# Kernel tuning notes

Hardware: AMD Instinct MI355X
Metric: run time of the kernel (lower is better)

The kernel has to match this reference:

```python
import jax, jax.numpy as jnp
import numpy as np

LN_EPS = 1e-5
MIN_BW, MAX_BW, BW_FACTOR = 0.1, 10.0, 1.0
BETA = 0.1


def _layernorm(h, g, b):
    mu = jnp.mean(h, axis=-1, keepdims=True)
    var = jnp.mean((h - mu) ** 2, axis=-1, keepdims=True)
    return (h - mu) * jax.lax.rsqrt(var + LN_EPS) * g + b


def _mlp(x, W1, b1, g, beta, W2, b2):
    # Linear -> LayerNorm -> Dropout(eval: identity) -> GELU(exact) -> Linear
    h = x @ W1 + b1
    h = _layernorm(h, g, beta)
    h = jax.nn.gelu(h, approximate=False)
    return h @ W2 + b2


def _normalize(x):
    n = jnp.linalg.norm(x, axis=-1, keepdims=True)
    return x / jnp.maximum(n, 1e-12)


def _bandwidth(x, y):
    # median-heuristic bandwidth on up to 512 samples; no grad through it
    s = min(512, x.shape[0])
    xs, ys = x[:s], y[:s]
    diff = xs[:, None, :] - ys[None, :, :]          # [s, s, K]
    dist_sq = jnp.sum(diff ** 2, axis=-1)
    bw = jnp.sqrt(jnp.median(dist_sq.reshape(-1)) / 2.0) * BW_FACTOR
    return jax.lax.stop_gradient(jnp.clip(bw, MIN_BW, MAX_BW))


def _score_kernel(x, sx, y, sy):
    # 3-term KSD kernel matrix [B, B]
    bw = _bandwidth(x, y)
    bw2 = bw ** 2
    x2 = jnp.sum(x ** 2, axis=-1)
    y2 = jnp.sum(y ** 2, axis=-1)
    dist_sq = jnp.maximum(x2[:, None] + y2[None, :] - 2.0 * (x @ y.T), 0.0)
    k = jnp.exp(-dist_sq / (2.0 * bw2))
    term1 = k * (sx @ sy.T)
    # sum_d (x_i - y_j)_d * sy_jd  = x_i . sy_j - y_j . sy_j
    term2 = (x @ sy.T - jnp.sum(y * sy, axis=-1)[None, :]) * k / bw2
    D = x.shape[-1]
    term3 = dist_sq * k / (bw2 ** 2) - k * D / bw2
    return term1 + term2 + term3


def setup_inputs() -> dict:
    key = jax.random.key(0)
    B, L, D1, H, K = 256, 128, 768, 1024, 256
    ks = jax.random.split(key, 16)

    def w(k, shape):
        return (jax.random.normal(k, shape, dtype=jnp.float32) * 0.02)

    inp = {
        'image_features': jax.random.normal(ks[0], (B, L, D1), dtype=jnp.float32),
        'text_features': jax.random.normal(ks[1], (B, L, D1), dtype=jnp.float32),
        'eps_img': jax.random.normal(ks[2], (B, L, K), dtype=jnp.float32),
        'eps_txt': jax.random.normal(ks[3], (B, L, K), dtype=jnp.float32),
        'attention_mask': jnp.ones((B, L), dtype=jnp.int32),
    }
    # encoders: D1 -> H -> 2K ; score nets: K -> 2K -> K
    for pfx, k1, k2 in (('enc_i', ks[4], ks[5]), ('enc_t', ks[6], ks[7])):
        inp[pfx + '_W1'] = w(k1, (D1, H)); inp[pfx + '_b1'] = jnp.zeros((H,), jnp.float32)
        inp[pfx + '_g'] = jnp.ones((H,), jnp.float32); inp[pfx + '_beta'] = jnp.zeros((H,), jnp.float32)
        inp[pfx + '_W2'] = w(k2, (H, 2 * K)); inp[pfx + '_b2'] = jnp.zeros((2 * K,), jnp.float32)
    for pfx, k1, k2 in (('sc_i', ks[8], ks[9]), ('sc_t', ks[10], ks[11])):
        inp[pfx + '_W1'] = w(k1, (K, 2 * K)); inp[pfx + '_b1'] = jnp.zeros((2 * K,), jnp.float32)
        inp[pfx + '_g'] = jnp.ones((2 * K,), jnp.float32); inp[pfx + '_beta'] = jnp.zeros((2 * K,), jnp.float32)
        inp[pfx + '_W2'] = w(k2, (2 * K, K)); inp[pfx + '_b2'] = jnp.zeros((K,), jnp.float32)
    return inp


def reference(image_features, text_features, attention_mask, eps_img, eps_txt,
              enc_i_W1, enc_i_b1, enc_i_g, enc_i_beta, enc_i_W2, enc_i_b2,
              enc_t_W1, enc_t_b1, enc_t_g, enc_t_beta, enc_t_W2, enc_t_b2,
              sc_i_W1, sc_i_b1, sc_i_g, sc_i_beta, sc_i_W2, sc_i_b2,
              sc_t_W1, sc_t_b1, sc_t_g, sc_t_beta, sc_t_W2, sc_t_b2):
    B = image_features.shape[0]
    img_params = _mlp(image_features, enc_i_W1, enc_i_b1, enc_i_g, enc_i_beta, enc_i_W2, enc_i_b2)
    txt_params = _mlp(text_features, enc_t_W1, enc_t_b1, enc_t_g, enc_t_beta, enc_t_W2, enc_t_b2)
    K = img_params.shape[-1] // 2
    img_mu, img_logvar = img_params[..., :K], img_params[..., K:]
    txt_mu, txt_logvar = txt_params[..., :K], txt_params[..., K:]

    img_z = _normalize(img_mu + eps_img * jnp.exp(0.5 * img_logvar))
    txt_z = _normalize(txt_mu + eps_txt * jnp.exp(0.5 * txt_logvar))

    img_score = _mlp(img_z, sc_i_W1, sc_i_b1, sc_i_g, sc_i_beta, sc_i_W2, sc_i_b2)
    txt_score = _mlp(txt_z, sc_t_W1, sc_t_b1, sc_t_g, sc_t_beta, sc_t_W2, sc_t_b2)

    seq_last = jnp.sum(attention_mask, axis=1).astype(jnp.int32) - 1   # [B]
    bidx = jnp.arange(B)
    xz, yz = img_z[bidx, seq_last], txt_z[bidx, seq_last]
    xs, ys = img_score[bidx, seq_last], txt_score[bidx, seq_last]

    alignment_loss = jnp.mean(_score_kernel(xz, xs, yz, ys))

    kl1 = -0.5 * jnp.sum(1.0 + img_logvar - img_mu ** 2 - jnp.exp(img_logvar), axis=-1)
    kl2 = -0.5 * jnp.sum(1.0 + txt_logvar - txt_mu ** 2 - jnp.exp(txt_logvar), axis=-1)
    kl_loss = (jnp.mean(kl1[bidx, seq_last]) + jnp.mean(kl2[bidx, seq_last])) / 2.0

    total_loss = kl_loss + BETA * alignment_loss
    return total_loss
```

## Files before the change

### kernel.cpp

```cpp
#include <hip/hip_runtime.h>
#include <math.h>

#define Bb   256
#define Lq   128
#define D1   768
#define Hh   1024
#define Kk   256
#define K2v  512

#define OFF_EPSG  0
#define OFF_P     131072
#define OFF_Z     2228224
#define OFF_SCORE 2359296
#define OFF_DIST  2490368
#define OFF_HIST  2555904
#define OFF_SCAL  2564096
#define OFF_YSY   2564104
#define OFF_SEQL  2564616
#define OFF_BF    2564880

#define UB_XG   0
#define UB_HACT 393216
#define UB_ZB   917504
#define UB_WT   1048576
#define WT_EW1I 0
#define WT_EW1T 786432
#define WT_EW2I 1572864
#define WT_EW2T 2097152
#define WT_SW1I 2621440
#define WT_SW1T 2752512
#define WT_SW2I 2883584
#define WT_SW2T 3014656

typedef __attribute__((ext_vector_type(8))) short short8v;
typedef __attribute__((ext_vector_type(4))) float f32x4;

__device__ __forceinline__ float wred(float v){
#pragma unroll
  for (int m = 32; m; m >>= 1) v += __shfl_xor(v, m, 64);
  return v;
}
__device__ __forceinline__ float gelu_exact(float x){
  return 0.5f * x * (1.0f + erff(x * 0.70710678118654752f));
}
__device__ __forceinline__ ushort f2b(float f){
  union { float f; unsigned u; } v; v.f = f;
  return (ushort)((v.u + 0x7FFFu + ((v.u >> 16) & 1u)) >> 16);
}

__global__ __launch_bounds__(256) void k_init(const int* __restrict__ mask,
                                              int* __restrict__ seql,
                                              int* __restrict__ ghist,
                                              float* __restrict__ scal){
  const int t = threadIdx.x, b = blockIdx.x;
  if (b == 0){
    const int4* m4 = reinterpret_cast<const int4*>(mask + t * Lq);
    int s = 0;
#pragma unroll
    for (int i = 0; i < Lq/4; i++){ int4 v = m4[i]; s += v.x + v.y + v.z + v.w; }
    seql[t] = s - 1;
  } else {
    reinterpret_cast<int4*>(ghist)[(b-1)*256 + t] = make_int4(0,0,0,0);
    if (b == 1 && t < 8) scal[t] = 0.0f;
  }
}

__global__ __launch_bounds__(256) void k_gather_conv(
    const float* __restrict__ img, const float* __restrict__ txt,
    const float* __restrict__ epsi, const float* __restrict__ epst,
    const int* __restrict__ seql,
    const float* __restrict__ eW1i, const float* __restrict__ eW1t,
    const float* __restrict__ eW2i, const float* __restrict__ eW2t,
    const float* __restrict__ sW1i, const float* __restrict__ sW1t,
    const float* __restrict__ sW2i, const float* __restrict__ sW2t,
    ushort* __restrict__ xgb, float* __restrict__ epsg, ushort* __restrict__ wt)
{
  __shared__ float lsf[32][33];
  const int bid = blockIdx.x, t = threadIdx.x;
  if (bid < 256){
    const int b = bid, last = seql[b];
    const float4* ir = reinterpret_cast<const float4*>(img + (size_t)(b*Lq+last)*D1);
    const float4* tr = reinterpret_cast<const float4*>(txt + (size_t)(b*Lq+last)*D1);
    if (t < 192){
      float4 v = ir[t];
      ushort4 o; o.x=f2b(v.x); o.y=f2b(v.y); o.z=f2b(v.z); o.w=f2b(v.w);
      reinterpret_cast<ushort4*>(xgb + (size_t)b*D1)[t] = o;
      float4 w = tr[t];
      ushort4 p; p.x=f2b(w.x); p.y=f2b(w.y); p.z=f2b(w.z); p.w=f2b(w.w);
      reinterpret_cast<ushort4*>(xgb + (size_t)(Bb+b)*D1)[t] = p;
    }
    if (t < 64){
      reinterpret_cast<float4*>(epsg + (size_t)b*Kk)[t] =
        reinterpret_cast<const float4*>(epsi + (size_t)(b*Lq+last)*Kk)[t];
      reinterpret_cast<float4*>(epsg + (size_t)(Bb+b)*Kk)[t] =
        reinterpret_cast<const float4*>(epst + (size_t)(b*Lq+last)*Kk)[t];
    }
    return;
  }
  const int wb = bid - 256;
  const float* src; ushort* dst; int Kd, Nd, ti;
  if      (wb < 768){  src=eW1i; dst=wt+WT_EW1I; Kd=768;  Nd=1024; ti=wb; }
  else if (wb < 1536){ src=eW1t; dst=wt+WT_EW1T; Kd=768;  Nd=1024; ti=wb-768; }
  else if (wb < 2048){ src=eW2i; dst=wt+WT_EW2I; Kd=1024; Nd=512;  ti=wb-1536; }
  else if (wb < 2560){ src=eW2t; dst=wt+WT_EW2T; Kd=1024; Nd=512;  ti=wb-2048; }
  else if (wb < 2688){ src=sW1i; dst=wt+WT_SW1I; Kd=256;  Nd=512;  ti=wb-2560; }
  else if (wb < 2816){ src=sW1t; dst=wt+WT_SW1T; Kd=256;  Nd=512;  ti=wb-2688; }
  else if (wb < 2944){ src=sW2i; dst=wt+WT_SW2I; Kd=512;  Nd=256;  ti=wb-2816; }
  else               { src=sW2t; dst=wt+WT_SW2T; Kd=512;  Nd=256;  ti=wb-2944; }
  const int ntile = Nd / 32;
  const int k0 = (ti / ntile) * 32, n0 = (ti % ntile) * 32;
  const int r = t >> 3, q = t & 7;
  float4 v = reinterpret_cast<const float4*>(src + (size_t)(k0+r)*Nd + n0)[q];
  lsf[r][q*4+0]=v.x; lsf[r][q*4+1]=v.y; lsf[r][q*4+2]=v.z; lsf[r][q*4+3]=v.w;
  __syncthreads();
  ushort4 o;
  o.x = f2b(lsf[q*4+0][r]); o.y = f2b(lsf[q*4+1][r]);
  o.z = f2b(lsf[q*4+2][r]); o.w = f2b(lsf[q*4+3][r]);
  *reinterpret_cast<ushort4*>(dst + (size_t)(n0+r)*Kd + k0 + q*4) = o;
}

template<int BM, int KCH, int N, int K>
__global__ __launch_bounds__(256) void k_mgemm(
    const ushort* __restrict__ A, const ushort* __restrict__ WTi,
    const ushort* __restrict__ WTt, float* __restrict__ P)
{
  constexpr int RPW = BM / 64;
  __shared__ ushort LS[(BM + 64) * 32];
  const int tid = threadIdx.x;
  const int lane = tid & 63, wid = tid >> 6;
  const int n0 = blockIdx.x * 64;
  const int r0 = blockIdx.y * BM;
  const int kb = blockIdx.z * KCH;
  const ushort* WT = (r0 >= 256) ? WTt : WTi;

  f32x4 acc[RPW][4];
#pragma unroll
  for (int s = 0; s < RPW; s++)
#pragma unroll
    for (int c = 0; c < 4; c++) acc[s][c] = (f32x4){0.f,0.f,0.f,0.f};

  const int l15 = lane & 15, kg = lane >> 4;
  const int rdswz = (kg * 16) ^ ((l15 & 3) << 4);

  for (int k0 = kb; k0 < kb + KCH; k0 += 32){
    __syncthreads();
    constexpr int NCHK = (BM + 64) * 4;
#pragma unroll
    for (int i = 0; i < NCHK / 256; i++){
      const int q = (i * 256 + tid) * 16;
      const int row = q >> 6, koff = q & 63;
      const ushort* src = (row < BM)
          ? (A  + (size_t)(r0 + row) * K + k0)
          : (WT + (size_t)(n0 + row - BM) * K + k0);
      short8v v = *reinterpret_cast<const short8v*>(
          reinterpret_cast<const char*>(src) + koff);
      const int dq = (q & ~63) | (koff ^ ((row & 3) << 4));
      *reinterpret_cast<short8v*>(reinterpret_cast<char*>(LS) + dq) = v;
    }
    __syncthreads();
    const char* Ab = reinterpret_cast<const char*>(LS);
    const char* Bbp = reinterpret_cast<const char*>(LS + BM * 32);
    short8v ar[RPW], bc[4];
#pragma unroll
    for (int s = 0; s < RPW; s++){
      const int row = wid * (RPW * 16) + s * 16 + l15;
      ar[s] = *reinterpret_cast<const short8v*>(Ab + row * 64 + rdswz);
    }
#pragma unroll
    for (int c = 0; c < 4; c++){
      const int col = c * 16 + l15;
      bc[c] = *reinterpret_cast<const short8v*>(Bbp + col * 64 + rdswz);
    }
#pragma unroll
    for (int s = 0; s < RPW; s++)
#pragma unroll
      for (int c = 0; c < 4; c++)
        acc[s][c] = __builtin_amdgcn_mfma_f32_16x16x32_bf16(ar[s], bc[c], acc[s][c], 0, 0, 0);
  }
  const int ks = blockIdx.z;
#pragma unroll
  for (int s = 0; s < RPW; s++)
#pragma unroll
    for (int c = 0; c < 4; c++)
#pragma unroll
      for (int r = 0; r < 4; r++){
        const int row = r0 + wid * (RPW * 16) + s * 16 + kg * 4 + r;
        const int col = n0 + c * 16 + l15;
        P[((size_t)ks * 512 + row) * N + col] = acc[s][c][r];
      }
}

__global__ __launch_bounds__(256) void k_ln1(
    const float* __restrict__ P,
    const float* __restrict__ b1i, const float* __restrict__ b1t,
    const float* __restrict__ gi,  const float* __restrict__ gt,
    const float* __restrict__ bei, const float* __restrict__ bet,
    ushort* __restrict__ hb)
{
  __shared__ float2 wsum[4];
  const int row = blockIdx.x, t = threadIdx.x;
  const float* b1 = row >= 256 ? b1t : b1i;
  const float* g  = row >= 256 ? gt  : gi;
  const float* be = row >= 256 ? bet : bei;
  const float4* P4 = reinterpret_cast<const float4*>(P);
  float4 v = make_float4(0,0,0,0);
#pragma unroll
  for (int s = 0; s < 4; s++){
    float4 p = P4[((size_t)s * 512 + row) * (Hh/4) + t];
    v.x += p.x; v.y += p.y; v.z += p.z; v.w += p.w;
  }
  float4 bb = reinterpret_cast<const float4*>(b1)[t];
  v.x += bb.x; v.y += bb.y; v.z += bb.z; v.w += bb.w;
  float ps = wred(v.x + v.y + v.z + v.w);
  float pq = wred(v.x*v.x + v.y*v.y + v.z*v.z + v.w*v.w);
  if (!(t & 63)) wsum[t >> 6] = make_float2(ps, pq);
  __syncthreads();
  float S = 0, Q = 0;
#pragma unroll
  for (int i = 0; i < 4; i++){ S += wsum[i].x; Q += wsum[i].y; }
  float mean = S * (1.0f/Hh);
  float rstd = rsqrtf(Q * (1.0f/Hh) - mean*mean + 1e-5f);
  float4 gv  = reinterpret_cast<const float4*>(g)[t];
  float4 bev = reinterpret_cast<const float4*>(be)[t];
  ushort4 o;
  o.x = f2b(gelu_exact((v.x - mean)*rstd*gv.x + bev.x));
  o.y = f2b(gelu_exact((v.y - mean)*rstd*gv.y + bev.y));
  o.z = f2b(gelu_exact((v.z - mean)*rstd*gv.z + bev.z));
  o.w = f2b(gelu_exact((v.w - mean)*rstd*gv.w + bev.w));
  reinterpret_cast<ushort4*>(hb)[(size_t)row * 256 + t] = o;
}

__global__ __launch_bounds__(128) void k_ln2(
    const float* __restrict__ P,
    const float* __restrict__ b1i, const float* __restrict__ b1t,
    const float* __restrict__ gi,  const float* __restrict__ gt,
    const float* __restrict__ bei, const float* __restrict__ bet,
    ushort* __restrict__ hb2)
{
  __shared__ float2 wsum[2];
  const int row = blockIdx.x, t = threadIdx.x;
  const float* b1 = row >= 256 ? b1t : b1i;
  const float* g  = row >= 256 ? gt  : gi;
  const float* be = row >= 256 ? bet : bei;
  const float4* P4 = reinterpret_cast<const float4*>(P);
  float4 v = make_float4(0,0,0,0);
#pragma unroll
  for (int s = 0; s < 4; s++){
    float4 p = P4[((size_t)s * 512 + row) * (K2v/4) + t];
    v.x += p.x; v.y += p.y; v.z += p.z; v.w += p.w;
  }
  float4 bb = reinterpret_cast<const float4*>(b1)[t];
  v.x += bb.x; v.y += bb.y; v.z += bb.z; v.w += bb.w;
  float ps = wred(v.x + v.y + v.z + v.w);
  float pq = wred(v.x*v.x + v.y*v.y + v.z*v.z + v.w*v.w);
  if (!(t & 63)) wsum[t >> 6] = make_float2(ps, pq);
  __syncthreads();
  float S = wsum[0].x + wsum[1].x, Q = wsum[0].y + wsum[1].y;
  float mean = S * (1.0f/K2v);
  float rstd = rsqrtf(Q * (1.0f/K2v) - mean*mean + 1e-5f);
  float4 gv  = reinterpret_cast<const float4*>(g)[t];
  float4 bev = reinterpret_cast<const float4*>(be)[t];
  ushort4 o;
  o.x = f2b(gelu_exact((v.x - mean)*rstd*gv.x + bev.x));
  o.y = f2b(gelu_exact((v.y - mean)*rstd*gv.y + bev.y));
  o.z = f2b(gelu_exact((v.z - mean)*rstd*gv.z + bev.z));
  o.w = f2b(gelu_exact((v.w - mean)*rstd*gv.w + bev.w));
  reinterpret_cast<ushort4*>(hb2)[(size_t)row * 128 + t] = o;
}

__global__ __launch_bounds__(64) void k_reparam(
    const float* __restrict__ P,
    const float* __restrict__ b2i, const float* __restrict__ b2t,
    const float* __restrict__ epsg, float* __restrict__ z,
    ushort* __restrict__ zb, float* __restrict__ kl)
{
  const int row = blockIdx.x, t = threadIdx.x;
  const float* b2 = row >= 256 ? b2t : b2i;
  const float4* P4 = reinterpret_cast<const float4*>(P);
  float4 mu = make_float4(0,0,0,0), lv = make_float4(0,0,0,0);
#pragma unroll
  for (int s = 0; s < 8; s++){
    float4 a = P4[((size_t)s * 512 + row) * (K2v/4) + t];
    float4 c = P4[((size_t)s * 512 + row) * (K2v/4) + 64 + t];
    mu.x += a.x; mu.y += a.y; mu.z += a.z; mu.w += a.w;
    lv.x += c.x; lv.y += c.y; lv.z += c.z; lv.w += c.w;
  }
  float4 bm = reinterpret_cast<const float4*>(b2)[t];
  float4 bl = reinterpret_cast<const float4*>(b2)[64 + t];
  mu.x += bm.x; mu.y += bm.y; mu.z += bm.z; mu.w += bm.w;
  lv.x += bl.x; lv.y += bl.y; lv.z += bl.z; lv.w += bl.w;
  float4 ev = reinterpret_cast<const float4*>(epsg)[(size_t)row * 64 + t];
  float z0 = mu.x + ev.x * expf(0.5f * lv.x);
  float z1 = mu.y + ev.y * expf(0.5f * lv.y);
  float z2 = mu.z + ev.z * expf(0.5f * lv.z);
  float z3 = mu.w + ev.w * expf(0.5f * lv.w);
  float s2 = wred(z0*z0 + z1*z1 + z2*z2 + z3*z3);
  float klp = (1.0f + lv.x - mu.x*mu.x - expf(lv.x))
            + (1.0f + lv.y - mu.y*mu.y - expf(lv.y))
            + (1.0f + lv.z - mu.z*mu.z - expf(lv.z))
            + (1.0f + lv.w - mu.w*mu.w - expf(lv.w));
  float klt = wred(klp);
  float inv = 1.0f / fmaxf(sqrtf(s2), 1e-12f);
  float4 zv = make_float4(z0*inv, z1*inv, z2*inv, z3*inv);
  reinterpret_cast<float4*>(z)[(size_t)row * 64 + t] = zv;
  ushort4 o; o.x=f2b(zv.x); o.y=f2b(zv.y); o.z=f2b(zv.z); o.w=f2b(zv.w);
  reinterpret_cast<ushort4*>(zb)[(size_t)row * 64 + t] = o;
  if (t == 0) atomicAdd(kl + (row >= 256 ? 1 : 0), -0.5f * klt);
}

__global__ __launch_bounds__(64) void k_sum2(
    const float* __restrict__ P,
    const float* __restrict__ b2i, const float* __restrict__ b2t,
    const float* __restrict__ z, float* __restrict__ score, float* __restrict__ ysy)
{
  const int row = blockIdx.x, t = threadIdx.x;
  const float* b2 = row >= 256 ? b2t : b2i;
  const float4* P4 = reinterpret_cast<const float4*>(P);
  float4 v = make_float4(0,0,0,0);
#pragma unroll
  for (int s = 0; s < 8; s++){
    float4 p = P4[((size_t)s * 512 + row) * (Kk/4) + t];
    v.x += p.x; v.y += p.y; v.z += p.z; v.w += p.w;
  }
  float4 bb = reinterpret_cast<const float4*>(b2)[t];
  v.x += bb.x; v.y += bb.y; v.z += bb.z; v.w += bb.w;
  reinterpret_cast<float4*>(score)[(size_t)row * 64 + t] = v;
  float4 zv = reinterpret_cast<const float4*>(z)[(size_t)row * 64 + t];
  float yp = wred(zv.x*v.x + zv.y*v.y + zv.z*v.z + zv.w*v.w);
  if (t == 0) ysy[row] = yp;
}

__global__ __launch_bounds__(256) void k_dist(const float* __restrict__ z,
                                              float* __restrict__ dist, int* __restrict__ ghist){
  __shared__ __align__(16) float xsh[Kk];
  __shared__ int hl[8192];
  const int i = blockIdx.x, j = threadIdx.x;
  xsh[j] = z[(size_t)i * Kk + j];
#pragma unroll
  for (int k = j; k < 8192; k += 256) hl[k] = 0;
  __syncthreads();
  const float4* y4 = reinterpret_cast<const float4*>(z + (size_t)Bb * Kk);
  const float4* x4 = reinterpret_cast<const float4*>(xsh);
  float acc = 0.0f;
#pragma unroll 4
  for (int d = 0; d < Kk; d += 4){
    float4 xv = x4[d >> 2];
    float4 yv = y4[j * (Kk/4) + (d >> 2)];
    float d0 = xv.x - yv.x, d1 = xv.y - yv.y, d2 = xv.z - yv.z, d3 = xv.w - yv.w;
    acc += d0*d0 + d1*d1 + d2*d2 + d3*d3;
  }
  dist[i * 256 + j] = acc;
  int bin = (int)(acc * 2048.0f);
  bin = bin < 0 ? 0 : (bin > 8191 ? 8191 : bin);
  atomicAdd(&hl[bin], 1);
  __syncthreads();
  for (int k = j; k < 8192; k += 256){
    int c = hl[k];
    if (c) atomicAdd(ghist + k, c);
  }
}

__global__ __launch_bounds__(256) void k_score(
    const float* __restrict__ z, const float* __restrict__ score,
    const float* __restrict__ dist, const float* __restrict__ ysy,
    const int* __restrict__ ghist, float* __restrict__ scal,
    float* __restrict__ out)
{
  __shared__ __align__(16) float xsh[Kk];
  __shared__ __align__(16) float sxsh[Kk];
  __shared__ int wt4[4];
  __shared__ int bres[2];
  __shared__ float red4[4];
  __shared__ float s_bw2;
  const int i = blockIdx.x, j = threadIdx.x;
  xsh[j]  = z[(size_t)i * Kk + j];
  sxsh[j] = score[(size_t)i * Kk + j];

  {
    const int lane = j & 63, w = j >> 6;
    const int base = j * 32;
    int s = 0;
#pragma unroll
    for (int u = 0; u < 32; u++) s += ghist[base + u];
    int sc = s;
#pragma unroll
    for (int m = 1; m < 64; m <<= 1){
      int o = __shfl_up(sc, m, 64);
      if (lane >= m) sc += o;
    }
    if (lane == 63) wt4[w] = sc;
    __syncthreads();
    int off = 0;
    for (int q = 0; q < w; q++) off += wt4[q];
    int cum = sc + off, basex = cum - s;
#pragma unroll
    for (int rr = 0; rr < 2; rr++){
      int rank = 32768 + rr;
      if (basex < rank && cum >= rank){
        int c = basex;
        for (int u = 0; u < 32; u++){
          c += ghist[base + u];
          if (c >= rank){ bres[rr] = base + u; break; }
        }
      }
    }
    __syncthreads();
    if (j == 0){
      float med = 0.5f * ((bres[0] + 0.5f) + (bres[1] + 0.5f)) * (1.0f / 2048.0f);
      float bw = sqrtf(med * 0.5f);
      bw = fminf(fmaxf(bw, 0.1f), 10.0f);
      s_bw2 = bw * bw;
    }
    __syncthreads();
  }
  const float bw2 = s_bw2;
  const float4* sy4 = reinterpret_cast<const float4*>(score + (size_t)Bb * Kk);
  const float4* x4  = reinterpret_cast<const float4*>(xsh);
  const float4* sx4 = reinterpret_cast<const float4*>(sxsh);
  float ssy = 0, xsy = 0;
#pragma unroll 4
  for (int d = 0; d < Kk; d += 4){
    float4 xv  = x4[d >> 2];
    float4 sxv = sx4[d >> 2];
    float4 syv = sy4[j * (Kk/4) + (d >> 2)];
    ssy += sxv.x*syv.x + sxv.y*syv.y + sxv.z*syv.z + sxv.w*syv.w;
    xsy += xv.x*syv.x + xv.y*syv.y + xv.z*syv.z + xv.w*syv.w;
  }
  float d2 = dist[i * 256 + j];
  float kv = expf(-d2 / (2.0f * bw2));
  float t1 = kv * ssy;
  float t2 = (xsy - ysy[Bb + j]) * kv / bw2;
  float t3 = d2 * kv / (bw2 * bw2) - kv * (float)Kk / bw2;
  float s = wred(t1 + t2 + t3);
  if (!(j & 63)) red4[j >> 6] = s;
  __syncthreads();
  if (j == 0){
    atomicAdd(scal + 2, red4[0] + red4[1] + red4[2] + red4[3]);
    __threadfence();
    int old = atomicAdd(reinterpret_cast<int*>(scal + 4), 1);
    if (old == 255){
      float kli = __int_as_float(atomicAdd(reinterpret_cast<int*>(scal + 0), 0));
      float klt = __int_as_float(atomicAdd(reinterpret_cast<int*>(scal + 1), 0));
      float alg = __int_as_float(atomicAdd(reinterpret_cast<int*>(scal + 2), 0));
      out[0] = 0.5f * (kli + klt) * (1.0f/256.0f) + 0.1f * alg * (1.0f/65536.0f);
    }
  }
}

extern "C" void kernel_launch(void* const* d_in, const int* in_sizes, int n_in,
                              void* d_out, int out_size, void* d_ws, size_t ws_size,
                              hipStream_t stream) {
  (void)in_sizes; (void)n_in; (void)out_size; (void)ws_size;
  const float* img  = (const float*)d_in[0];
  const float* txt  = (const float*)d_in[1];
  const float* epsi = (const float*)d_in[2];
  const float* epst = (const float*)d_in[3];
  const int*   mask = (const int*)d_in[4];
  const float* eW1i = (const float*)d_in[5];
  const float* eb1i = (const float*)d_in[6];
  const float* egi  = (const float*)d_in[7];
  const float* ebei = (const float*)d_in[8];
  const float* eW2i = (const float*)d_in[9];
  const float* eb2i = (const float*)d_in[10];
  const float* eW1t = (const float*)d_in[11];
  const float* eb1t = (const float*)d_in[12];
  const float* egt  = (const float*)d_in[13];
  const float* ebet = (const float*)d_in[14];
  const float* eW2t = (const float*)d_in[15];
  const float* eb2t = (const float*)d_in[16];
  const float* sW1i = (const float*)d_in[17];
  const float* sb1i = (const float*)d_in[18];
  const float* sgi  = (const float*)d_in[19];
  const float* sbei = (const float*)d_in[20];
  const float* sW2i = (const float*)d_in[21];
  const float* sb2i = (const float*)d_in[22];
  const float* sW1t = (const float*)d_in[23];
  const float* sb1t = (const float*)d_in[24];
  const float* sgt  = (const float*)d_in[25];
  const float* sbet = (const float*)d_in[26];
  const float* sW2t = (const float*)d_in[27];
  const float* sb2t = (const float*)d_in[28];

  float*  ws    = (float*)d_ws;
  float*  epsg  = ws + OFF_EPSG;
  float*  P     = ws + OFF_P;
  float*  z     = ws + OFF_Z;
  float*  score = ws + OFF_SCORE;
  float*  dist  = ws + OFF_DIST;
  int*    ghist = (int*)(ws + OFF_HIST);
  float*  scal  = ws + OFF_SCAL;
  float*  ysy   = ws + OFF_YSY;
  int*    seql  = (int*)(ws + OFF_SEQL);
  ushort* ub    = (ushort*)(ws + OFF_BF);
  ushort* xgb   = ub + UB_XG;
  ushort* hb    = ub + UB_HACT;
  ushort* zb    = ub + UB_ZB;
  ushort* wt    = ub + UB_WT;

  k_init<<<9, 256, 0, stream>>>(mask, seql, ghist, scal);
  k_gather_conv<<<3328, 256, 0, stream>>>(img, txt, epsi, epst, seql,
                                          eW1i, eW1t, eW2i, eW2t,
                                          sW1i, sW1t, sW2i, sW2t,
                                          xgb, epsg, wt);
  k_mgemm<128,192,1024,768><<<dim3(16,4,4), 256, 0, stream>>>(xgb, wt+WT_EW1I, wt+WT_EW1T, P);
  k_ln1<<<512, 256, 0, stream>>>(P, eb1i, eb1t, egi, egt, ebei, ebet, hb);
  k_mgemm<128,128,512,1024><<<dim3(8,4,8), 256, 0, stream>>>(hb, wt+WT_EW2I, wt+WT_EW2T, P);
  k_reparam<<<512, 64, 0, stream>>>(P, eb2i, eb2t, epsg, z, zb, scal);
  k_mgemm<64,64,512,256><<<dim3(8,8,4), 256, 0, stream>>>(zb, wt+WT_SW1I, wt+WT_SW1T, P);
  k_ln2<<<512, 128, 0, stream>>>(P, sb1i, sb1t, sgi, sgt, sbei, sbet, hb);
  k_mgemm<64,64,256,512><<<dim3(4,8,8), 256, 0, stream>>>(hb, wt+WT_SW2I, wt+WT_SW2T, P);
  k_sum2<<<512, 64, 0, stream>>>(P, sb2i, sb2t, z, score, ysy);

  k_dist<<<256, 256, 0, stream>>>(z, dist, ghist);
  k_score<<<256, 256, 0, stream>>>(z, score, dist, ysy, ghist, scal, (float*)d_out);
}
```

Before: 94.94 us.

## Fuse small kernels, co-schedule score GEMM with distance pass, deepen split-K

Merges the mask-length/init kernel into the gather/convert kernel, runs the first score-net GEMM and the pairwise distance/histogram pass as separate block ranges of one launch, and moves the median-bandwidth computation into the score-sum kernel so it is computed once rather than in every score block. Split-K depth is doubled for the encoder and second score GEMMs, with workspace offsets enlarged to hold the extra partials. This cuts launch count and redundant bandwidth work and raises GEMM parallelism, at the cost of more partial-sum traffic in the reduction kernels.

```diff
diff --git a/kernel.cpp b/kernel.cpp
--- a/kernel.cpp
+++ b/kernel.cpp
@@ -10,14 +10,13 @@
 
 #define OFF_EPSG  0
 #define OFF_P     131072
-#define OFF_Z     2228224
-#define OFF_SCORE 2359296
-#define OFF_DIST  2490368
-#define OFF_HIST  2555904
-#define OFF_SCAL  2564096
-#define OFF_YSY   2564104
-#define OFF_SEQL  2564616
-#define OFF_BF    2564880
+#define OFF_Z     4325376
+#define OFF_SCORE 4456448
+#define OFF_DIST  4587520
+#define OFF_HIST  4653056
+#define OFF_SCAL  4661248
+#define OFF_YSY   4661256
+#define OFF_BF    4661768
 
 #define UB_XG   0
 #define UB_HACT 393216
@@ -40,6 +39,11 @@
   for (int m = 32; m; m >>= 1) v += __shfl_xor(v, m, 64);
   return v;
 }
+__device__ __forceinline__ int wredi(int v){
+#pragma unroll
+  for (int m = 32; m; m >>= 1) v += __shfl_xor(v, m, 64);
+  return v;
+}
 __device__ __forceinline__ float gelu_exact(float x){
   return 0.5f * x * (1.0f + erff(x * 0.70710678118654752f));
 }
@@ -48,52 +52,124 @@
   return (ushort)((v.u + 0x7FFFu + ((v.u >> 16) & 1u)) >> 16);
 }
 
-__global__ __launch_bounds__(256) void k_init(const int* __restrict__ mask,
-                                              int* __restrict__ seql,
-                                              int* __restrict__ ghist,
-                                              float* __restrict__ scal){
-  const int t = threadIdx.x, b = blockIdx.x;
-  if (b == 0){
-    const int4* m4 = reinterpret_cast<const int4*>(mask + t * Lq);
-    int s = 0;
-#pragma unroll
-    for (int i = 0; i < Lq/4; i++){ int4 v = m4[i]; s += v.x + v.y + v.z + v.w; }
-    seql[t] = s - 1;
-  } else {
-    reinterpret_cast<int4*>(ghist)[(b-1)*256 + t] = make_int4(0,0,0,0);
-    if (b == 1 && t < 8) scal[t] = 0.0f;
-  }
-}
-
-__global__ __launch_bounds__(256) void k_gather_conv(
+template<int BM,int KCH,int N,int K>
+__device__ __forceinline__ void gemm_stage(
+    const ushort* __restrict__ A, const ushort* __restrict__ WTi,
+    const ushort* __restrict__ WTt, float* __restrict__ P,
+    ushort* LS, int tid, int n0, int r0, int kb, int ks)
+{
+  constexpr int RPW = BM / 64;
+  const int lane = tid & 63, wid = tid >> 6;
+  const ushort* WT = (r0 >= 256) ? WTt : WTi;
+
+  f32x4 acc[RPW][4];
+#pragma unroll
+  for (int s = 0; s < RPW; s++)
+#pragma unroll
+    for (int c = 0; c < 4; c++) acc[s][c] = (f32x4){0.f,0.f,0.f,0.f};
+
+  const int l15 = lane & 15, kg = lane >> 4;
+  const int rdswz = (kg * 16) ^ ((l15 & 3) << 4);
+
+  for (int k0 = kb; k0 < kb + KCH; k0 += 32){
+    __syncthreads();
+    constexpr int NCHK = (BM + 64) * 4;
+#pragma unroll
+    for (int i = 0; i < NCHK / 256; i++){
+      const int q = (i * 256 + tid) * 16;
+      const int row = q >> 6, koff = q & 63;
+      const ushort* src = (row < BM)
+          ? (A  + (size_t)(r0 + row) * K + k0)
+          : (WT + (size_t)(n0 + row - BM) * K + k0);
+      short8v v = *reinterpret_cast<const short8v*>(
+          reinterpret_cast<const char*>(src) + koff);
+      const int dq = (q & ~63) | (koff ^ ((row & 3) << 4));
+      *reinterpret_cast<short8v*>(reinterpret_cast<char*>(LS) + dq) = v;
+    }
+    __syncthreads();
+    const char* Ab  = reinterpret_cast<const char*>(LS);
+    const char* Bbp = reinterpret_cast<const char*>(LS + BM * 32);
+    short8v ar[RPW], bc[4];
+#pragma unroll
+    for (int s = 0; s < RPW; s++){
+      const int row = wid * (RPW * 16) + s * 16 + l15;
+      ar[s] = *reinterpret_cast<const short8v*>(Ab + row * 64 + rdswz);
+    }
+#pragma unroll
+    for (int c = 0; c < 4; c++){
+      const int col = c * 16 + l15;
+      bc[c] = *reinterpret_cast<const short8v*>(Bbp + col * 64 + rdswz);
+    }
+#pragma unroll
+    for (int s = 0; s < RPW; s++)
+#pragma unroll
+      for (int c = 0; c < 4; c++)
+        acc[s][c] = __builtin_amdgcn_mfma_f32_16x16x32_bf16(ar[s], bc[c], acc[s][c], 0, 0, 0);
+  }
+#pragma unroll
+  for (int s = 0; s < RPW; s++)
+#pragma unroll
+    for (int c = 0; c < 4; c++)
+#pragma unroll
+      for (int r = 0; r < 4; r++){
+        const int row = r0 + wid * (RPW * 16) + s * 16 + kg * 4 + r;
+        const int col = n0 + c * 16 + l15;
+        P[((size_t)ks * 512 + row) * N + col] = acc[s][c][r];
+      }
+}
+
+template<int BM,int KCH,int N,int K>
+__global__ __launch_bounds__(256) void k_mgemm(
+    const ushort* __restrict__ A, const ushort* __restrict__ WTi,
+    const ushort* __restrict__ WTt, float* __restrict__ P)
+{
+  __shared__ __align__(16) ushort LS[(BM + 64) * 32];
+  gemm_stage<BM,KCH,N,K>(A, WTi, WTt, P, LS, threadIdx.x,
+                         blockIdx.x * 64, blockIdx.y * BM,
+                         blockIdx.z * KCH, blockIdx.z);
+}
+
+__global__ __launch_bounds__(256) void k_prep(
     const float* __restrict__ img, const float* __restrict__ txt,
     const float* __restrict__ epsi, const float* __restrict__ epst,
-    const int* __restrict__ seql,
+    const int* __restrict__ mask,
     const float* __restrict__ eW1i, const float* __restrict__ eW1t,
     const float* __restrict__ eW2i, const float* __restrict__ eW2t,
     const float* __restrict__ sW1i, const float* __restrict__ sW1t,
     const float* __restrict__ sW2i, const float* __restrict__ sW2t,
-    ushort* __restrict__ xgb, float* __restrict__ epsg, ushort* __restrict__ wt)
+    ushort* __restrict__ xgb, float* __restrict__ epsg, ushort* __restrict__ wt,
+    int* __restrict__ ghist, float* __restrict__ scal)
 {
   __shared__ float lsf[32][33];
+  __shared__ int s_last;
   const int bid = blockIdx.x, t = threadIdx.x;
   if (bid < 256){
-    const int b = bid, last = seql[b];
-    const float4* ir = reinterpret_cast<const float4*>(img + (size_t)(b*Lq+last)*D1);
-    const float4* tr = reinterpret_cast<const float4*>(txt + (size_t)(b*Lq+last)*D1);
+    if (t < 8) reinterpret_cast<int4*>(ghist)[bid * 8 + t] = make_int4(0,0,0,0);
+    if (bid == 0 && t < 8) scal[t] = 0.0f;
+    int s = 0;
+    if (t < 32){
+      int4 v = reinterpret_cast<const int4*>(mask + bid * Lq)[t];
+      s = v.x + v.y + v.z + v.w;
+    }
+    if (t < 64){
+      int tot = wredi(s);
+      if (t == 0) s_last = tot - 1;
+    }
+    __syncthreads();
+    const int last = s_last;
     if (t < 192){
-      float4 v = ir[t];
+      float4 v = reinterpret_cast<const float4*>(img + (size_t)(bid*Lq+last)*D1)[t];
       ushort4 o; o.x=f2b(v.x); o.y=f2b(v.y); o.z=f2b(v.z); o.w=f2b(v.w);
-      reinterpret_cast<ushort4*>(xgb + (size_t)b*D1)[t] = o;
-      float4 w = tr[t];
-      ushort4 p; p.x=f2b(w.x); p.y=f2b(w.y); p.z=f2b(w.z); p.w=f2b(w.w);
-      reinterpret_cast<ushort4*>(xgb + (size_t)(Bb+b)*D1)[t] = p;
+      reinterpret_cast<ushort4*>(xgb + (size_t)bid*D1)[t] = o;
+      float4 w = reinterpret_cast<const float4*>(txt + (size_t)(bid*Lq+last)*D1)[t];
+      ushort4 q; q.x=f2b(w.x); q.y=f2b(w.y); q.z=f2b(w.z); q.w=f2b(w.w);
+      reinterpret_cast<ushort4*>(xgb + (size_t)(Bb+bid)*D1)[t] = q;
     }
     if (t < 64){
-      reinterpret_cast<float4*>(epsg + (size_t)b*Kk)[t] =
-        reinterpret_cast<const float4*>(epsi + (size_t)(b*Lq+last)*Kk)[t];
-      reinterpret_cast<float4*>(epsg + (size_t)(Bb+b)*Kk)[t] =
-        reinterpret_cast<const float4*>(epst + (size_t)(b*Lq+last)*Kk)[t];
+      reinterpret_cast<float4*>(epsg + (size_t)bid*Kk)[t] =
+        reinterpret_cast<const float4*>(epsi + (size_t)(bid*Lq+last)*Kk)[t];
+      reinterpret_cast<float4*>(epsg + (size_t)(Bb+bid)*Kk)[t] =
+        reinterpret_cast<const float4*>(epst + (size_t)(bid*Lq+last)*Kk)[t];
     }
     return;
   }
@@ -119,77 +195,7 @@
   *reinterpret_cast<ushort4*>(dst + (size_t)(n0+r)*Kd + k0 + q*4) = o;
 }
 
-template<int BM, int KCH, int N, int K>
-__global__ __launch_bounds__(256) void k_mgemm(
-    const ushort* __restrict__ A, const ushort* __restrict__ WTi,
-    const ushort* __restrict__ WTt, float* __restrict__ P)
-{
-  constexpr int RPW = BM / 64;
-  __shared__ ushort LS[(BM + 64) * 32];
-  const int tid = threadIdx.x;
-  const int lane = tid & 63, wid = tid >> 6;
-  const int n0 = blockIdx.x * 64;
-  const int r0 = blockIdx.y * BM;
-  const int kb = blockIdx.z * KCH;
-  const ushort* WT = (r0 >= 256) ? WTt : WTi;
-
-  f32x4 acc[RPW][4];
-#pragma unroll
-  for (int s = 0; s < RPW; s++)
-#pragma unroll
-    for (int c = 0; c < 4; c++) acc[s][c] = (f32x4){0.f,0.f,0.f,0.f};
-
-  const int l15 = lane & 15, kg = lane >> 4;
-  const int rdswz = (kg * 16) ^ ((l15 & 3) << 4);
-
-  for (int k0 = kb; k0 < kb + KCH; k0 += 32){
-    __syncthreads();
-    constexpr int NCHK = (BM + 64) * 4;
-#pragma unroll
-    for (int i = 0; i < NCHK / 256; i++){
-      const int q = (i * 256 + tid) * 16;
-      const int row = q >> 6, koff = q & 63;
-      const ushort* src = (row < BM)
-          ? (A  + (size_t)(r0 + row) * K + k0)
-          : (WT + (size_t)(n0 + row - BM) * K + k0);
-      short8v v = *reinterpret_cast<const short8v*>(
-          reinterpret_cast<const char*>(src) + koff);
-      const int dq = (q & ~63) | (koff ^ ((row & 3) << 4));
-      *reinterpret_cast<short8v*>(reinterpret_cast<char*>(LS) + dq) = v;
-    }
-    __syncthreads();
-    const char* Ab = reinterpret_cast<const char*>(LS);
-    const char* Bbp = reinterpret_cast<const char*>(LS + BM * 32);
-    short8v ar[RPW], bc[4];
-#pragma unroll
-    for (int s = 0; s < RPW; s++){
-      const int row = wid * (RPW * 16) + s * 16 + l15;
-      ar[s] = *reinterpret_cast<const short8v*>(Ab + row * 64 + rdswz);
-    }
-#pragma unroll
-    for (int c = 0; c < 4; c++){
-      const int col = c * 16 + l15;
-      bc[c] = *reinterpret_cast<const short8v*>(Bbp + col * 64 + rdswz);
-    }
-#pragma unroll
-    for (int s = 0; s < RPW; s++)
-#pragma unroll
-      for (int c = 0; c < 4; c++)
-        acc[s][c] = __builtin_amdgcn_mfma_f32_16x16x32_bf16(ar[s], bc[c], acc[s][c], 0, 0, 0);
-  }
-  const int ks = blockIdx.z;
-#pragma unroll
-  for (int s = 0; s < RPW; s++)
-#pragma unroll
-    for (int c = 0; c < 4; c++)
-#pragma unroll
-      for (int r = 0; r < 4; r++){
-        const int row = r0 + wid * (RPW * 16) + s * 16 + kg * 4 + r;
-        const int col = n0 + c * 16 + l15;
-        P[((size_t)ks * 512 + row) * N + col] = acc[s][c][r];
-      }
-}
-
+template<int NS>
 __global__ __launch_bounds__(256) void k_ln1(
     const float* __restrict__ P,
     const float* __restrict__ b1i, const float* __restrict__ b1t,
@@ -205,7 +211,7 @@
   const float4* P4 = reinterpret_cast<const float4*>(P);
   float4 v = make_float4(0,0,0,0);
 #pragma unroll
-  for (int s = 0; s < 4; s++){
+  for (int s = 0; s < NS; s++){
     float4 p = P4[((size_t)s * 512 + row) * (Hh/4) + t];
     v.x += p.x; v.y += p.y; v.z += p.z; v.w += p.w;
   }
@@ -230,6 +236,7 @@
   reinterpret_cast<ushort4*>(hb)[(size_t)row * 256 + t] = o;
 }
 
+template<int NS>
 __global__ __launch_bounds__(128) void k_ln2(
     const float* __restrict__ P,
     const float* __restrict__ b1i, const float* __restrict__ b1t,
@@ -245,7 +252,7 @@
   const float4* P4 = reinterpret_cast<const float4*>(P);
   float4 v = make_float4(0,0,0,0);
 #pragma unroll
-  for (int s = 0; s < 4; s++){
+  for (int s = 0; s < NS; s++){
     float4 p = P4[((size_t)s * 512 + row) * (K2v/4) + t];
     v.x += p.x; v.y += p.y; v.z += p.z; v.w += p.w;
   }
@@ -268,6 +275,7 @@
   reinterpret_cast<ushort4*>(hb2)[(size_t)row * 128 + t] = o;
 }
 
+template<int NS>
 __global__ __launch_bounds__(64) void k_reparam(
     const float* __restrict__ P,
     const float* __restrict__ b2i, const float* __restrict__ b2t,
@@ -279,7 +287,7 @@
   const float4* P4 = reinterpret_cast<const float4*>(P);
   float4 mu = make_float4(0,0,0,0), lv = make_float4(0,0,0,0);
 #pragma unroll
-  for (int s = 0; s < 8; s++){
+  for (int s = 0; s < NS; s++){
     float4 a = P4[((size_t)s * 512 + row) * (K2v/4) + t];
     float4 c = P4[((size_t)s * 512 + row) * (K2v/4) + 64 + t];
     mu.x += a.x; mu.y += a.y; mu.z += a.z; mu.w += a.w;
@@ -308,33 +316,24 @@
   if (t == 0) atomicAdd(kl + (row >= 256 ? 1 : 0), -0.5f * klt);
 }
 
-__global__ __launch_bounds__(64) void k_sum2(
-    const float* __restrict__ P,
-    const float* __restrict__ b2i, const float* __restrict__ b2t,
-    const float* __restrict__ z, float* __restrict__ score, float* __restrict__ ysy)
-{
-  const int row = blockIdx.x, t = threadIdx.x;
-  const float* b2 = row >= 256 ? b2t : b2i;
-  const float4* P4 = reinterpret_cast<const float4*>(P);
-  float4 v = make_float4(0,0,0,0);
-#pragma unroll
-  for (int s = 0; s < 8; s++){
-    float4 p = P4[((size_t)s * 512 + row) * (Kk/4) + t];
-    v.x += p.x; v.y += p.y; v.z += p.z; v.w += p.w;
-  }
-  float4 bb = reinterpret_cast<const float4*>(b2)[t];
-  v.x += bb.x; v.y += bb.y; v.z += bb.z; v.w += bb.w;
-  reinterpret_cast<float4*>(score)[(size_t)row * 64 + t] = v;
-  float4 zv = reinterpret_cast<const float4*>(z)[(size_t)row * 64 + t];
-  float yp = wred(zv.x*v.x + zv.y*v.y + zv.z*v.z + zv.w*v.w);
-  if (t == 0) ysy[row] = yp;
-}
-
-__global__ __launch_bounds__(256) void k_dist(const float* __restrict__ z,
-                                              float* __restrict__ dist, int* __restrict__ ghist){
-  __shared__ __align__(16) float xsh[Kk];
-  __shared__ int hl[8192];
-  const int i = blockIdx.x, j = threadIdx.x;
+__global__ __launch_bounds__(256) void k_sc1dist(
+    const ushort* __restrict__ zb, const ushort* __restrict__ WTi,
+    const ushort* __restrict__ WTt, float* __restrict__ P,
+    const float* __restrict__ z, float* __restrict__ dist, int* __restrict__ ghist)
+{
+  __shared__ __align__(16) char SM[256*4 + 8192*4];
+  const int bid = blockIdx.x, t = threadIdx.x;
+  if (bid < 256){
+    ushort* LS = reinterpret_cast<ushort*>(SM);
+    const int n0 = (bid & 7) * 64;
+    const int r0 = ((bid >> 3) & 7) * 64;
+    const int ks = bid >> 6;
+    gemm_stage<64,64,512,256>(zb, WTi, WTt, P, LS, t, n0, r0, ks * 64, ks);
+    return;
+  }
+  float* xsh = reinterpret_cast<float*>(SM);
+  int*   hl  = reinterpret_cast<int*>(SM + 1024);
+  const int i = bid - 256, j = t;
   xsh[j] = z[(size_t)i * Kk + j];
 #pragma unroll
   for (int k = j; k < 8192; k += 256) hl[k] = 0;
@@ -360,60 +359,83 @@
   }
 }
 
+template<int NS>
+__global__ __launch_bounds__(256) void k_sum2bw(
+    const float* __restrict__ P,
+    const float* __restrict__ b2i, const float* __restrict__ b2t,
+    const float* __restrict__ z, float* __restrict__ score, float* __restrict__ ysy,
+    const int* __restrict__ ghist, float* __restrict__ scal)
+{
+  const int bid = blockIdx.x, t = threadIdx.x;
+  if (bid < 128){
+    const int row = bid * 4 + (t >> 6), lane = t & 63;
+    const float* b2 = row >= 256 ? b2t : b2i;
+    const float4* P4 = reinterpret_cast<const float4*>(P);
+    float4 v = make_float4(0,0,0,0);
+#pragma unroll
+    for (int s = 0; s < NS; s++){
+      float4 q = P4[((size_t)s * 512 + row) * (Kk/4) + lane];
+      v.x += q.x; v.y += q.y; v.z += q.z; v.w += q.w;
+    }
+    float4 bb = reinterpret_cast<const float4*>(b2)[lane];
+    v.x += bb.x; v.y += bb.y; v.z += bb.z; v.w += bb.w;
+    reinterpret_cast<float4*>(score)[(size_t)row * 64 + lane] = v;
+    float4 zv = reinterpret_cast<const float4*>(z)[(size_t)row * 64 + lane];
+    float yp = wred(zv.x*v.x + zv.y*v.y + zv.z*v.z + zv.w*v.w);
+    if (lane == 0) ysy[row] = yp;
+    return;
+  }
+  __shared__ int wt4[4];
+  __shared__ int bres[2];
+  const int lane = t & 63, w = t >> 6;
+  const int base = t * 32;
+  int s = 0;
+#pragma unroll
+  for (int u = 0; u < 32; u++) s += ghist[base + u];
+  int sc = s;
+#pragma unroll
+  for (int m = 1; m < 64; m <<= 1){
+    int o = __shfl_up(sc, m, 64);
+    if (lane >= m) sc += o;
+  }
+  if (lane == 63) wt4[w] = sc;
+  __syncthreads();
+  int off = 0;
+  for (int q = 0; q < w; q++) off += wt4[q];
+  int cum = sc + off, basex = cum - s;
+#pragma unroll
+  for (int rr = 0; rr < 2; rr++){
+    int rank = 32768 + rr;
+    if (basex < rank && cum >= rank){
+      int c = basex;
+      for (int u = 0; u < 32; u++){
+        c += ghist[base + u];
+        if (c >= rank){ bres[rr] = base + u; break; }
+      }
+    }
+  }
+  __syncthreads();
+  if (t == 0){
+    float med = 0.5f * ((bres[0] + 0.5f) + (bres[1] + 0.5f)) * (1.0f / 2048.0f);
+    float bw = sqrtf(med * 0.5f);
+    bw = fminf(fmaxf(bw, 0.1f), 10.0f);
+    scal[3] = bw * bw;
+  }
+}
+
 __global__ __launch_bounds__(256) void k_score(
     const float* __restrict__ z, const float* __restrict__ score,
     const float* __restrict__ dist, const float* __restrict__ ysy,
-    const int* __restrict__ ghist, float* __restrict__ scal,
-    float* __restrict__ out)
+    float* __restrict__ scal, float* __restrict__ out)
 {
   __shared__ __align__(16) float xsh[Kk];
   __shared__ __align__(16) float sxsh[Kk];
-  __shared__ int wt4[4];
-  __shared__ int bres[2];
   __shared__ float red4[4];
-  __shared__ float s_bw2;
   const int i = blockIdx.x, j = threadIdx.x;
   xsh[j]  = z[(size_t)i * Kk + j];
   sxsh[j] = score[(size_t)i * Kk + j];
-
-  {
-    const int lane = j & 63, w = j >> 6;
-    const int base = j * 32;
-    int s = 0;
-#pragma unroll
-    for (int u = 0; u < 32; u++) s += ghist[base + u];
-    int sc = s;
-#pragma unroll
-    for (int m = 1; m < 64; m <<= 1){
-      int o = __shfl_up(sc, m, 64);
-      if (lane >= m) sc += o;
-    }
-    if (lane == 63) wt4[w] = sc;
-    __syncthreads();
-    int off = 0;
-    for (int q = 0; q < w; q++) off += wt4[q];
-    int cum = sc + off, basex = cum - s;
-#pragma unroll
-    for (int rr = 0; rr < 2; rr++){
-      int rank = 32768 + rr;
-      if (basex < rank && cum >= rank){
-        int c = basex;
-        for (int u = 0; u < 32; u++){
-          c += ghist[base + u];
-          if (c >= rank){ bres[rr] = base + u; break; }
-        }
-      }
-    }
-    __syncthreads();
-    if (j == 0){
-      float med = 0.5f * ((bres[0] + 0.5f) + (bres[1] + 0.5f)) * (1.0f / 2048.0f);
-      float bw = sqrtf(med * 0.5f);
-      bw = fminf(fmaxf(bw, 0.1f), 10.0f);
-      s_bw2 = bw * bw;
-    }
-    __syncthreads();
-  }
-  const float bw2 = s_bw2;
+  __syncthreads();
+  const float bw2 = scal[3];
   const float4* sy4 = reinterpret_cast<const float4*>(score + (size_t)Bb * Kk);
   const float4* x4  = reinterpret_cast<const float4*>(xsh);
   const float4* sx4 = reinterpret_cast<const float4*>(sxsh);
@@ -490,27 +512,23 @@
   int*    ghist = (int*)(ws + OFF_HIST);
   float*  scal  = ws + OFF_SCAL;
   float*  ysy   = ws + OFF_YSY;
-  int*    seql  = (int*)(ws + OFF_SEQL);
   ushort* ub    = (ushort*)(ws + OFF_BF);
   ushort* xgb   = ub + UB_XG;
   ushort* hb    = ub + UB_HACT;
   ushort* zb    = ub + UB_ZB;
   ushort* wt    = ub + UB_WT;
 
-  k_init<<<9, 256, 0, stream>>>(mask, seql, ghist, scal);
-  k_gather_conv<<<3328, 256, 0, stream>>>(img, txt, epsi, epst, seql,
-                                          eW1i, eW1t, eW2i, eW2t,
-                                          sW1i, sW1t, sW2i, sW2t,
-                                          xgb, epsg, wt);
-  k_mgemm<128,192,1024,768><<<dim3(16,4,4), 256, 0, stream>>>(xgb, wt+WT_EW1I, wt+WT_EW1T, P);
-  k_ln1<<<512, 256, 0, stream>>>(P, eb1i, eb1t, egi, egt, ebei, ebet, hb);
-  k_mgemm<128,128,512,1024><<<dim3(8,4,8), 256, 0, stream>>>(hb, wt+WT_EW2I, wt+WT_EW2T, P);
-  k_reparam<<<512, 64, 0, stream>>>(P, eb2i, eb2t, epsg, z, zb, scal);
-  k_mgemm<64,64,512,256><<<dim3(8,8,4), 256, 0, stream>>>(zb, wt+WT_SW1I, wt+WT_SW1T, P);
-  k_ln2<<<512, 128, 0, stream>>>(P, sb1i, sb1t, sgi, sgt, sbei, sbet, hb);
-  k_mgemm<64,64,256,512><<<dim3(4,8,8), 256, 0, stream>>>(hb, wt+WT_SW2I, wt+WT_SW2T, P);
-  k_sum2<<<512, 64, 0, stream>>>(P, sb2i, sb2t, z, score, ysy);
-
-  k_dist<<<256, 256, 0, stream>>>(z, dist, ghist);
-  k_score<<<256, 256, 0, stream>>>(z, score, dist, ysy, ghist, scal, (float*)d_out);
-}
+  k_prep<<<3328, 256, 0, stream>>>(img, txt, epsi, epst, mask,
+                                   eW1i, eW1t, eW2i, eW2t,
+                                   sW1i, sW1t, sW2i, sW2t,
+                                   xgb, epsg, wt, ghist, scal);
+  k_mgemm<128,96,1024,768><<<dim3(16,4,8), 256, 0, stream>>>(xgb, wt+WT_EW1I, wt+WT_EW1T, P);
+  k_ln1<8><<<512, 256, 0, stream>>>(P, eb1i, eb1t, egi, egt, ebei, ebet, hb);
+  k_mgemm<128,64,512,1024><<<dim3(8,4,16), 256, 0, stream>>>(hb, wt+WT_EW2I, wt+WT_EW2T, P);
+  k_reparam<16><<<512, 64, 0, stream>>>(P, eb2i, eb2t, epsg, z, zb, scal);
+  k_sc1dist<<<512, 256, 0, stream>>>(zb, wt+WT_SW1I, wt+WT_SW1T, P, z, dist, ghist);
+  k_ln2<4><<<512, 128, 0, stream>>>(P, sb1i, sb1t, sgi, sgt, sbei, sbet, hb);
+  k_mgemm<64,32,256,512><<<dim3(4,8,16), 256, 0, stream>>>(hb, wt+WT_SW2I, wt+WT_SW2T, P);
+  k_sum2bw<16><<<129, 256, 0, stream>>>(P, sb2i, sb2t, z, score, ysy, ghist, scal);
+  k_score<<<256, 256, 0, stream>>>(z, score, dist, ysy, scal, (float*)d_out);
+}
```

Measured after the change: 94.48 us. Within noise of the previous version (-0.5%).
